# Performance work log

Measured on AMD Instinct MI355X. Metric: run time of the kernel, lower is better.

Reference implementation:

```python
import jax, jax.numpy as jnp
import numpy as np

B, D_IN, D_CTX, UNITS, RANK = 4096, 2048, 512, 2048, 256


def setup_inputs() -> dict:
    key = jax.random.key(0)
    ks = jax.random.split(key, 6)
    scale_u = 1.0 / np.sqrt(D_IN)
    scale_w = 1.0 / np.sqrt(D_CTX)
    return {
        "inputs": jax.random.normal(ks[0], (B, D_IN), dtype=jnp.float32),
        "context": jax.random.normal(ks[1], (B, D_CTX), dtype=jnp.float32),
        "U": jax.random.normal(ks[2], (D_IN, RANK), dtype=jnp.float32) * scale_u,
        "S": jax.random.uniform(ks[3], (RANK,), dtype=jnp.float32) + 0.5,
        "V": jax.random.normal(ks[4], (UNITS, RANK), dtype=jnp.float32) * scale_u,
        "W": jax.random.normal(ks[5], (D_CTX, RANK), dtype=jnp.float32) * scale_w,
        "Bc": jnp.zeros((RANK,), dtype=jnp.float32),
        "bias": jnp.zeros((UNITS,), dtype=jnp.float32),
    }


def reference(inputs, context, U, S, V, W, Bc, bias):
    # h = context @ W + Bc ; chi = sigmoid(h) ; s[b,r] = S[r] * chi[b,r]
    chi = jax.nn.sigmoid(context @ W + Bc)           # [B, R]
    s = S * chi                                       # [B, R]
    # Original math: out[b,m] = sum_{n,r} x[b,n] U[n,r] s[b,r] V[m,r]
    # Reassociated (identical math, no [B,N,M] kernel): ((x @ U) * s) @ V^T
    proj = (inputs @ U) * s                           # [B, R]
    out = proj @ V.T + bias                           # [B, UNITS]
    return out  # activation is linear (None)
```

## Files before the change

kernel.cpp:

```cpp
#include <hip/hip_runtime.h>
#include <math.h>

namespace {

constexpr int Bdim  = 4096;
constexpr int D_IN  = 2048;
constexpr int D_CTX = 512;
constexpr int UNITS = 2048;
constexpr int RANK  = 256;
constexpr int SPLIT = 8;

typedef __bf16 bf16x8 __attribute__((ext_vector_type(8)));
typedef float  f32x4  __attribute__((ext_vector_type(4)));

__global__ __launch_bounds__(256) void k_prep(
    const float* __restrict__ U, const float* __restrict__ W,
    __bf16* __restrict__ Ut, __bf16* __restrict__ Wt) {
  const int job = blockIdx.y;
  const int t = threadIdx.x;
  const float* src = job ? W : U;
  __bf16* dst      = job ? Wt : Ut;
  const int K = job ? D_CTX : D_IN;
  const int tilesK = K / 64;
  const int tid = blockIdx.x;
  if (tid >= tilesK * 4) return;
  const int k0 = (tid % tilesK) * 64;
  const int n0 = (tid / tilesK) * 64;
  __shared__ __bf16 T[64][72];
  const int i  = t >> 4;
  const int j4 = (t & 15) * 4;
  for (int ii = i; ii < 64; ii += 16) {
    float4 v = *(const float4*)(src + (size_t)(k0 + ii) * RANK + n0 + j4);
    T[j4 + 0][ii] = (__bf16)v.x;
    T[j4 + 1][ii] = (__bf16)v.y;
    T[j4 + 2][ii] = (__bf16)v.z;
    T[j4 + 3][ii] = (__bf16)v.w;
  }
  __syncthreads();
  const int jj = t >> 3;
  const int c  = t & 7;
  for (int j2 = jj; j2 < 64; j2 += 32) {
    bf16x8 v = *(const bf16x8*)&T[j2][c * 8];
    *(bf16x8*)(dst + (size_t)(n0 + j2) * K + k0 + c * 8) = v;
  }
}

template <int BM, int BN, int BK, int WAVES_M, int WAVES_N,
          bool A_F32, bool B_F32, int EPI>
__global__ __launch_bounds__(256) void gemm_bt(
    const void* __restrict__ Ap, const void* __restrict__ Btp,
    void* __restrict__ Cp, const float* __restrict__ e0,
    const float* __restrict__ e1, const __bf16* __restrict__ part_in,
    int Mt, int Nt, int Kt, int kchunk) {
  constexpr int FM = BM / WAVES_M / 16;
  constexpr int FN = BN / WAVES_N / 16;
  constexpr int ACH = BM * 8 / 256;
  constexpr int BCH = BN * 8 / 256;
  static_assert(WAVES_M * WAVES_N == 4, "4 waves");
  static_assert(BK == 64, "row = 128B");
  static_assert(ACH >= 1 && BCH >= 1, "chunking");
  static_assert(EPI != 4 || (BM * BN * 4 <= BN * BK * 2), "red fits in Bs");
  __shared__ __align__(16) __bf16 As[BM * BK];
  __shared__ __align__(16) __bf16 Bs[BN * BK];
  const int t  = threadIdx.x;
  const int bm = blockIdx.x * BM;
  const int bn = (EPI == 3) ? 0 : blockIdx.y * BN;
  const int k_lo = (EPI == 3) ? blockIdx.y * kchunk : 0;
  const int k_hi = (EPI == 3) ? k_lo + kchunk : Kt;
  const int w = t >> 6, l = t & 63;
  const int wr0 = (w / WAVES_N) * (FM * 16);
  const int wc0 = (w % WAVES_N) * (FN * 16);
  const int lrow = l & 15;
  const int lk   = l >> 4;
  f32x4 acc[FM][FN] = {};

  float4 a_lo[ACH], a_hi[ACH];
  bf16x8 a_bf[ACH];
  float4 b_lo[BCH], b_hi[BCH];
  bf16x8 b_bf[BCH];

  auto LOADA = [&](int k0) {
#pragma unroll
    for (int ci = 0; ci < ACH; ++ci) {
      const int c = t + ci * 256;
      const int row = c >> 3, kc = c & 7;
      if constexpr (A_F32) {
        const float* g = (const float*)Ap + (size_t)(bm + row) * Kt + k0 + kc * 8;
        a_lo[ci] = *(const float4*)g;
        a_hi[ci] = *(const float4*)(g + 4);
      } else {
        a_bf[ci] = *(const bf16x8*)((const __bf16*)Ap +
                                    (size_t)(bm + row) * Kt + k0 + kc * 8);
      }
    }
  };
  auto LOADB = [&](int k0) {
#pragma unroll
    for (int ci = 0; ci < BCH; ++ci) {
      const int c = t + ci * 256;
      const int row = c >> 3, kc = c & 7;
      if constexpr (B_F32) {
        const float* g = (const float*)Btp + (size_t)(bn + row) * Kt + k0 + kc * 8;
        b_lo[ci] = *(const float4*)g;
        b_hi[ci] = *(const float4*)(g + 4);
      } else {
        b_bf[ci] = *(const bf16x8*)((const __bf16*)Btp +
                                    (size_t)(bn + row) * Kt + k0 + kc * 8);
      }
    }
  };
  auto WRITEA = [&]() {
#pragma unroll
    for (int ci = 0; ci < ACH; ++ci) {
      const int c = t + ci * 256;
      const int row = c >> 3, kc = c & 7;
      bf16x8 v;
      if constexpr (A_F32) {
        v[0] = (__bf16)a_lo[ci].x; v[1] = (__bf16)a_lo[ci].y;
        v[2] = (__bf16)a_lo[ci].z; v[3] = (__bf16)a_lo[ci].w;
        v[4] = (__bf16)a_hi[ci].x; v[5] = (__bf16)a_hi[ci].y;
        v[6] = (__bf16)a_hi[ci].z; v[7] = (__bf16)a_hi[ci].w;
      } else {
        v = a_bf[ci];
      }
      *(bf16x8*)((char*)As + row * 128 + ((kc ^ (row & 7)) * 16)) = v;
    }
  };
  auto WRITEB = [&]() {
#pragma unroll
    for (int ci = 0; ci < BCH; ++ci) {
      const int c = t + ci * 256;
      const int row = c >> 3, kc = c & 7;
      bf16x8 v;
      if constexpr (B_F32) {
        v[0] = (__bf16)b_lo[ci].x; v[1] = (__bf16)b_lo[ci].y;
        v[2] = (__bf16)b_lo[ci].z; v[3] = (__bf16)b_lo[ci].w;
        v[4] = (__bf16)b_hi[ci].x; v[5] = (__bf16)b_hi[ci].y;
        v[6] = (__bf16)b_hi[ci].z; v[7] = (__bf16)b_hi[ci].w;
      } else {
        v = b_bf[ci];
      }
      *(bf16x8*)((char*)Bs + row * 128 + ((kc ^ (row & 7)) * 16)) = v;
    }
  };

  LOADA(k_lo);
  LOADB(k_lo);
  for (int k0 = k_lo; k0 < k_hi; k0 += BK) {
    WRITEA();
    WRITEB();
    __syncthreads();
    if (k0 + BK < k_hi) {
      LOADA(k0 + BK);
      LOADB(k0 + BK);
    }
#pragma unroll
    for (int kk = 0; kk < BK / 32; ++kk) {
      bf16x8 af[FM], bfr[FN];
#pragma unroll
      for (int mf = 0; mf < FM; ++mf) {
        const int row = wr0 + mf * 16 + lrow;
        af[mf] = *(const bf16x8*)((const char*)As + row * 128 +
                                  (((kk * 4 + lk) ^ (row & 7)) * 16));
      }
#pragma unroll
      for (int nf = 0; nf < FN; ++nf) {
        const int row = wc0 + nf * 16 + lrow;
        bfr[nf] = *(const bf16x8*)((const char*)Bs + row * 128 +
                                   (((kk * 4 + lk) ^ (row & 7)) * 16));
      }
#pragma unroll
      for (int mf = 0; mf < FM; ++mf)
#pragma unroll
        for (int nf = 0; nf < FN; ++nf)
          acc[mf][nf] = __builtin_amdgcn_mfma_f32_16x16x32_bf16(
              af[mf], bfr[nf], acc[mf][nf], 0, 0, 0);
    }
    __syncthreads();
  }

  float* red = (float*)Bs;
  if (EPI == 4) {
    const int row = t >> 3;
    const int ch  = (t & 7) * 8;
    float racc[8] = {};
    for (int sl = 0; sl < kchunk; ++sl) {
      bf16x8 v = *(const bf16x8*)(part_in +
                    ((size_t)sl * Mt + bm + row) * Nt + bn + ch);
#pragma unroll
      for (int i = 0; i < 8; ++i) racc[i] += (float)v[i];
    }
#pragma unroll
    for (int i = 0; i < 8; ++i) red[row * BN + ch + i] = racc[i];
    __syncthreads();
  }

#pragma unroll
  for (int mf = 0; mf < FM; ++mf) {
#pragma unroll
    for (int nf = 0; nf < FN; ++nf) {
#pragma unroll
      for (int r = 0; r < 4; ++r) {
        const int lm = wr0 + mf * 16 + lk * 4 + r;
        const int ln = wc0 + nf * 16 + lrow;
        const int m = bm + lm;
        const int n = bn + ln;
        const float val = acc[mf][nf][r];
        if (EPI == 2) {
          ((float*)Cp)[(size_t)m * Nt + n] = val + e0[n];
        } else if (EPI == 3) {
          ((__bf16*)Cp)[(size_t)blockIdx.y * Mt * Nt + (size_t)m * Nt + n] =
              (__bf16)val;
        } else {
          const float h    = val + e1[n];
          const float sval = e0[n] / (1.0f + __expf(-h));
          ((__bf16*)Cp)[(size_t)m * Nt + n] = (__bf16)(red[lm * BN + ln] * sval);
        }
      }
    }
  }
}

}

extern "C" void kernel_launch(void* const* d_in, const int* in_sizes, int n_in,
                              void* d_out, int out_size, void* d_ws, size_t ws_size,
                              hipStream_t stream) {
  const float* inputs  = (const float*)d_in[0];
  const float* context = (const float*)d_in[1];
  const float* U       = (const float*)d_in[2];
  const float* S       = (const float*)d_in[3];
  const float* V       = (const float*)d_in[4];
  const float* W       = (const float*)d_in[5];
  const float* Bc      = (const float*)d_in[6];
  const float* bias    = (const float*)d_in[7];
  float* out = (float*)d_out;

  char* ws = (char*)d_ws;
  __bf16* Ut   = (__bf16*)(ws);
  __bf16* Wt   = (__bf16*)(ws + 1048576);
  __bf16* proj = (__bf16*)(ws + 1310720);
  __bf16* part = (__bf16*)(ws + 3407872);

  k_prep<<<dim3(128, 2), 256, 0, stream>>>(U, W, Ut, Wt);

  gemm_bt<32, 256, 64, 1, 4, true, false, 3>
      <<<dim3(Bdim / 32, SPLIT), 256, 0, stream>>>(
      inputs, Ut, part, nullptr, nullptr, nullptr, Bdim, RANK, D_IN, D_IN / SPLIT);

  gemm_bt<32, 64, 64, 2, 2, true, false, 4>
      <<<dim3(Bdim / 32, RANK / 64), 256, 0, stream>>>(
      context, Wt, proj, S, Bc, part, Bdim, RANK, D_CTX, SPLIT);

  gemm_bt<128, 128, 64, 2, 2, false, true, 2>
      <<<dim3(Bdim / 128, UNITS / 128), 256, 0, stream>>>(
      proj, V, out, bias, nullptr, nullptr, Bdim, UNITS, RANK, 0);
}
```

Measured before the change: 49.73 us.

## Merge gate GEMM into split-K projection launch, add combine kernel, swizzle output tiles

Runs the context gate GEMM (context@W, sigmoid, times S) as an extra grid slice of the split-K projection kernel, so both GEMMs share one launch and execute concurrently. The gate writes s to a bf16 buffer, and a new elementwise kernel sums the split-K partials and multiplies by s to form proj. The output GEMM is specialised and gets a block-index swizzle for better L2 locality. In exchange the change adds an extra s buffer round-trip through memory and uses gate blocks that do 256-wide N tiles.

```diff
diff --git a/kernel.cpp b/kernel.cpp
--- a/kernel.cpp
+++ b/kernel.cpp
@@ -45,102 +45,60 @@
   }
 }
 
-template <int BM, int BN, int BK, int WAVES_M, int WAVES_N,
-          bool A_F32, bool B_F32, int EPI>
-__global__ __launch_bounds__(256) void gemm_bt(
-    const void* __restrict__ Ap, const void* __restrict__ Btp,
-    void* __restrict__ Cp, const float* __restrict__ e0,
-    const float* __restrict__ e1, const __bf16* __restrict__ part_in,
-    int Mt, int Nt, int Kt, int kchunk) {
-  constexpr int FM = BM / WAVES_M / 16;
-  constexpr int FN = BN / WAVES_N / 16;
-  constexpr int ACH = BM * 8 / 256;
-  constexpr int BCH = BN * 8 / 256;
-  static_assert(WAVES_M * WAVES_N == 4, "4 waves");
-  static_assert(BK == 64, "row = 128B");
-  static_assert(ACH >= 1 && BCH >= 1, "chunking");
-  static_assert(EPI != 4 || (BM * BN * 4 <= BN * BK * 2), "red fits in Bs");
+__global__ __launch_bounds__(256) void k_pg(
+    const float* __restrict__ x,   const __bf16* __restrict__ Ut,
+    const float* __restrict__ ctx, const __bf16* __restrict__ Wt,
+    const float* __restrict__ S,   const float* __restrict__ Bc,
+    __bf16* __restrict__ part, __bf16* __restrict__ s_out) {
+  constexpr int BM = 32, BN = 256, BK = 64;
   __shared__ __align__(16) __bf16 As[BM * BK];
   __shared__ __align__(16) __bf16 Bs[BN * BK];
-  const int t  = threadIdx.x;
+  const int t = threadIdx.x;
+  const bool gate = (blockIdx.y == 0);
+  const int slice = (int)blockIdx.y - 1;
   const int bm = blockIdx.x * BM;
-  const int bn = (EPI == 3) ? 0 : blockIdx.y * BN;
-  const int k_lo = (EPI == 3) ? blockIdx.y * kchunk : 0;
-  const int k_hi = (EPI == 3) ? k_lo + kchunk : Kt;
+  const float*  A = gate ? ctx : x;
+  const __bf16* B = gate ? Wt  : Ut;
+  const int Kt   = gate ? D_CTX : D_IN;
+  const int k_lo = gate ? 0 : slice * (D_IN / SPLIT);
+  const int k_hi = gate ? D_CTX : k_lo + (D_IN / SPLIT);
   const int w = t >> 6, l = t & 63;
-  const int wr0 = (w / WAVES_N) * (FM * 16);
-  const int wc0 = (w % WAVES_N) * (FN * 16);
+  const int wc0 = w * 64;
   const int lrow = l & 15;
   const int lk   = l >> 4;
-  f32x4 acc[FM][FN] = {};
-
-  float4 a_lo[ACH], a_hi[ACH];
-  bf16x8 a_bf[ACH];
-  float4 b_lo[BCH], b_hi[BCH];
-  bf16x8 b_bf[BCH];
+  f32x4 acc[2][4] = {};
+
+  float4 a_lo, a_hi;
+  bf16x8 b_bf[8];
+  const int srow = t >> 3, skc = t & 7;
 
   auto LOADA = [&](int k0) {
-#pragma unroll
-    for (int ci = 0; ci < ACH; ++ci) {
-      const int c = t + ci * 256;
-      const int row = c >> 3, kc = c & 7;
-      if constexpr (A_F32) {
-        const float* g = (const float*)Ap + (size_t)(bm + row) * Kt + k0 + kc * 8;
-        a_lo[ci] = *(const float4*)g;
-        a_hi[ci] = *(const float4*)(g + 4);
-      } else {
-        a_bf[ci] = *(const bf16x8*)((const __bf16*)Ap +
-                                    (size_t)(bm + row) * Kt + k0 + kc * 8);
-      }
-    }
+    const float* g = A + (size_t)(bm + srow) * Kt + k0 + skc * 8;
+    a_lo = *(const float4*)g;
+    a_hi = *(const float4*)(g + 4);
   };
   auto LOADB = [&](int k0) {
 #pragma unroll
-    for (int ci = 0; ci < BCH; ++ci) {
-      const int c = t + ci * 256;
-      const int row = c >> 3, kc = c & 7;
-      if constexpr (B_F32) {
-        const float* g = (const float*)Btp + (size_t)(bn + row) * Kt + k0 + kc * 8;
-        b_lo[ci] = *(const float4*)g;
-        b_hi[ci] = *(const float4*)(g + 4);
-      } else {
-        b_bf[ci] = *(const bf16x8*)((const __bf16*)Btp +
-                                    (size_t)(bn + row) * Kt + k0 + kc * 8);
-      }
+    for (int ci = 0; ci < 8; ++ci) {
+      const int c = t + ci * 256;
+      const int row = c >> 3, kc = c & 7;
+      b_bf[ci] = *(const bf16x8*)(B + (size_t)row * Kt + k0 + kc * 8);
     }
   };
   auto WRITEA = [&]() {
-#pragma unroll
-    for (int ci = 0; ci < ACH; ++ci) {
-      const int c = t + ci * 256;
-      const int row = c >> 3, kc = c & 7;
-      bf16x8 v;
-      if constexpr (A_F32) {
-        v[0] = (__bf16)a_lo[ci].x; v[1] = (__bf16)a_lo[ci].y;
-        v[2] = (__bf16)a_lo[ci].z; v[3] = (__bf16)a_lo[ci].w;
-        v[4] = (__bf16)a_hi[ci].x; v[5] = (__bf16)a_hi[ci].y;
-        v[6] = (__bf16)a_hi[ci].z; v[7] = (__bf16)a_hi[ci].w;
-      } else {
-        v = a_bf[ci];
-      }
-      *(bf16x8*)((char*)As + row * 128 + ((kc ^ (row & 7)) * 16)) = v;
-    }
+    bf16x8 v;
+    v[0] = (__bf16)a_lo.x; v[1] = (__bf16)a_lo.y;
+    v[2] = (__bf16)a_lo.z; v[3] = (__bf16)a_lo.w;
+    v[4] = (__bf16)a_hi.x; v[5] = (__bf16)a_hi.y;
+    v[6] = (__bf16)a_hi.z; v[7] = (__bf16)a_hi.w;
+    *(bf16x8*)((char*)As + srow * 128 + ((skc ^ (srow & 7)) * 16)) = v;
   };
   auto WRITEB = [&]() {
 #pragma unroll
-    for (int ci = 0; ci < BCH; ++ci) {
-      const int c = t + ci * 256;
-      const int row = c >> 3, kc = c & 7;
-      bf16x8 v;
-      if constexpr (B_F32) {
-        v[0] = (__bf16)b_lo[ci].x; v[1] = (__bf16)b_lo[ci].y;
-        v[2] = (__bf16)b_lo[ci].z; v[3] = (__bf16)b_lo[ci].w;
-        v[4] = (__bf16)b_hi[ci].x; v[5] = (__bf16)b_hi[ci].y;
-        v[6] = (__bf16)b_hi[ci].z; v[7] = (__bf16)b_hi[ci].w;
-      } else {
-        v = b_bf[ci];
-      }
-      *(bf16x8*)((char*)Bs + row * 128 + ((kc ^ (row & 7)) * 16)) = v;
+    for (int ci = 0; ci < 8; ++ci) {
+      const int c = t + ci * 256;
+      const int row = c >> 3, kc = c & 7;
+      *(bf16x8*)((char*)Bs + row * 128 + ((kc ^ (row & 7)) * 16)) = b_bf[ci];
     }
   };
 
@@ -155,67 +113,174 @@
       LOADB(k0 + BK);
     }
 #pragma unroll
-    for (int kk = 0; kk < BK / 32; ++kk) {
-      bf16x8 af[FM], bfr[FN];
-#pragma unroll
-      for (int mf = 0; mf < FM; ++mf) {
+    for (int kk = 0; kk < 2; ++kk) {
+      bf16x8 af[2], bfr[4];
+#pragma unroll
+      for (int mf = 0; mf < 2; ++mf) {
+        const int row = mf * 16 + lrow;
+        af[mf] = *(const bf16x8*)((const char*)As + row * 128 +
+                                  (((kk * 4 + lk) ^ (row & 7)) * 16));
+      }
+#pragma unroll
+      for (int nf = 0; nf < 4; ++nf) {
+        const int row = wc0 + nf * 16 + lrow;
+        bfr[nf] = *(const bf16x8*)((const char*)Bs + row * 128 +
+                                   (((kk * 4 + lk) ^ (row & 7)) * 16));
+      }
+#pragma unroll
+      for (int mf = 0; mf < 2; ++mf)
+#pragma unroll
+        for (int nf = 0; nf < 4; ++nf)
+          acc[mf][nf] = __builtin_amdgcn_mfma_f32_16x16x32_bf16(
+              af[mf], bfr[nf], acc[mf][nf], 0, 0, 0);
+    }
+    __syncthreads();
+  }
+
+#pragma unroll
+  for (int mf = 0; mf < 2; ++mf) {
+#pragma unroll
+    for (int nf = 0; nf < 4; ++nf) {
+#pragma unroll
+      for (int r = 0; r < 4; ++r) {
+        const int m = bm + mf * 16 + lk * 4 + r;
+        const int n = wc0 + nf * 16 + lrow;
+        const float val = acc[mf][nf][r];
+        if (gate) {
+          const float h = val + Bc[n];
+          s_out[(size_t)m * RANK + n] = (__bf16)(S[n] / (1.0f + __expf(-h)));
+        } else {
+          part[((size_t)slice * Bdim + m) * RANK + n] = (__bf16)val;
+        }
+      }
+    }
+  }
+}
+
+__global__ __launch_bounds__(256) void k_combine(
+    const __bf16* __restrict__ part, const __bf16* __restrict__ s,
+    __bf16* __restrict__ proj) {
+  const size_t i8 = ((size_t)blockIdx.x * 256 + threadIdx.x) * 8;
+  float sum[8] = {};
+#pragma unroll
+  for (int sl = 0; sl < SPLIT; ++sl) {
+    bf16x8 v = *(const bf16x8*)(part + (size_t)sl * Bdim * RANK + i8);
+#pragma unroll
+    for (int i = 0; i < 8; ++i) sum[i] += (float)v[i];
+  }
+  bf16x8 sv = *(const bf16x8*)(s + i8);
+  bf16x8 o;
+#pragma unroll
+  for (int i = 0; i < 8; ++i) o[i] = (__bf16)(sum[i] * (float)sv[i]);
+  *(bf16x8*)(proj + i8) = o;
+}
+
+__global__ __launch_bounds__(256) void k_out(
+    const __bf16* __restrict__ proj, const float* __restrict__ V,
+    const float* __restrict__ bias, float* __restrict__ out) {
+  constexpr int BM = 128, BN = 128, BK = 64;
+  constexpr int Kt = RANK;
+  __shared__ __align__(16) __bf16 As[BM * BK];
+  __shared__ __align__(16) __bf16 Bs[BN * BK];
+  const int t = threadIdx.x;
+  const int lin = (int)(blockIdx.y * gridDim.x + blockIdx.x);
+  const int swz = (lin & 7) * 64 + (lin >> 3);
+  const int bm = (swz & 31) * BM;
+  const int bn = (swz >> 5) * BN;
+  const int w = t >> 6, l = t & 63;
+  const int wr0 = (w >> 1) * 64;
+  const int wc0 = (w & 1) * 64;
+  const int lrow = l & 15;
+  const int lk   = l >> 4;
+  f32x4 acc[4][4] = {};
+
+  bf16x8 a_bf[4];
+  float4 b_lo[4], b_hi[4];
+
+  auto LOADA = [&](int k0) {
+#pragma unroll
+    for (int ci = 0; ci < 4; ++ci) {
+      const int c = t + ci * 256;
+      const int row = c >> 3, kc = c & 7;
+      a_bf[ci] = *(const bf16x8*)(proj + (size_t)(bm + row) * Kt + k0 + kc * 8);
+    }
+  };
+  auto LOADB = [&](int k0) {
+#pragma unroll
+    for (int ci = 0; ci < 4; ++ci) {
+      const int c = t + ci * 256;
+      const int row = c >> 3, kc = c & 7;
+      const float* g = V + (size_t)(bn + row) * Kt + k0 + kc * 8;
+      b_lo[ci] = *(const float4*)g;
+      b_hi[ci] = *(const float4*)(g + 4);
+    }
+  };
+  auto WRITEA = [&]() {
+#pragma unroll
+    for (int ci = 0; ci < 4; ++ci) {
+      const int c = t + ci * 256;
+      const int row = c >> 3, kc = c & 7;
+      *(bf16x8*)((char*)As + row * 128 + ((kc ^ (row & 7)) * 16)) = a_bf[ci];
+    }
+  };
+  auto WRITEB = [&]() {
+#pragma unroll
+    for (int ci = 0; ci < 4; ++ci) {
+      const int c = t + ci * 256;
+      const int row = c >> 3, kc = c & 7;
+      bf16x8 v;
+      v[0] = (__bf16)b_lo[ci].x; v[1] = (__bf16)b_lo[ci].y;
+      v[2] = (__bf16)b_lo[ci].z; v[3] = (__bf16)b_lo[ci].w;
+      v[4] = (__bf16)b_hi[ci].x; v[5] = (__bf16)b_hi[ci].y;
+      v[6] = (__bf16)b_hi[ci].z; v[7] = (__bf16)b_hi[ci].w;
+      *(bf16x8*)((char*)Bs + row * 128 + ((kc ^ (row & 7)) * 16)) = v;
+    }
+  };
+
+  LOADA(0);
+  LOADB(0);
+  for (int k0 = 0; k0 < Kt; k0 += BK) {
+    WRITEA();
+    WRITEB();
+    __syncthreads();
+    if (k0 + BK < Kt) {
+      LOADA(k0 + BK);
+      LOADB(k0 + BK);
+    }
+#pragma unroll
+    for (int kk = 0; kk < 2; ++kk) {
+      bf16x8 af[4], bfr[4];
+#pragma unroll
+      for (int mf = 0; mf < 4; ++mf) {
         const int row = wr0 + mf * 16 + lrow;
         af[mf] = *(const bf16x8*)((const char*)As + row * 128 +
                                   (((kk * 4 + lk) ^ (row & 7)) * 16));
       }
 #pragma unroll
-      for (int nf = 0; nf < FN; ++nf) {
+      for (int nf = 0; nf < 4; ++nf) {
         const int row = wc0 + nf * 16 + lrow;
         bfr[nf] = *(const bf16x8*)((const char*)Bs + row * 128 +
                                    (((kk * 4 + lk) ^ (row & 7)) * 16));
       }
 #pragma unroll
-      for (int mf = 0; mf < FM; ++mf)
-#pragma unroll
-        for (int nf = 0; nf < FN; ++nf)
+      for (int mf = 0; mf < 4; ++mf)
+#pragma unroll
+        for (int nf = 0; nf < 4; ++nf)
           acc[mf][nf] = __builtin_amdgcn_mfma_f32_16x16x32_bf16(
               af[mf], bfr[nf], acc[mf][nf], 0, 0, 0);
     }
     __syncthreads();
   }
 
-  float* red = (float*)Bs;
-  if (EPI == 4) {
-    const int row = t >> 3;
-    const int ch  = (t & 7) * 8;
-    float racc[8] = {};
-    for (int sl = 0; sl < kchunk; ++sl) {
-      bf16x8 v = *(const bf16x8*)(part_in +
-                    ((size_t)sl * Mt + bm + row) * Nt + bn + ch);
-#pragma unroll
-      for (int i = 0; i < 8; ++i) racc[i] += (float)v[i];
-    }
-#pragma unroll
-    for (int i = 0; i < 8; ++i) red[row * BN + ch + i] = racc[i];
-    __syncthreads();
-  }
-
-#pragma unroll
-  for (int mf = 0; mf < FM; ++mf) {
-#pragma unroll
-    for (int nf = 0; nf < FN; ++nf) {
+#pragma unroll
+  for (int mf = 0; mf < 4; ++mf) {
+#pragma unroll
+    for (int nf = 0; nf < 4; ++nf) {
 #pragma unroll
       for (int r = 0; r < 4; ++r) {
-        const int lm = wr0 + mf * 16 + lk * 4 + r;
-        const int ln = wc0 + nf * 16 + lrow;
-        const int m = bm + lm;
-        const int n = bn + ln;
-        const float val = acc[mf][nf][r];
-        if (EPI == 2) {
-          ((float*)Cp)[(size_t)m * Nt + n] = val + e0[n];
-        } else if (EPI == 3) {
-          ((__bf16*)Cp)[(size_t)blockIdx.y * Mt * Nt + (size_t)m * Nt + n] =
-              (__bf16)val;
-        } else {
-          const float h    = val + e1[n];
-          const float sval = e0[n] / (1.0f + __expf(-h));
-          ((__bf16*)Cp)[(size_t)m * Nt + n] = (__bf16)(red[lm * BN + ln] * sval);
-        }
+        const int m = bm + wr0 + mf * 16 + lk * 4 + r;
+        const int n = bn + wc0 + nf * 16 + lrow;
+        out[(size_t)m * UNITS + n] = acc[mf][nf][r] + bias[n];
       }
     }
   }
@@ -240,19 +305,15 @@
   __bf16* Ut   = (__bf16*)(ws);
   __bf16* Wt   = (__bf16*)(ws + 1048576);
   __bf16* proj = (__bf16*)(ws + 1310720);
-  __bf16* part = (__bf16*)(ws + 3407872);
+  __bf16* sbuf = (__bf16*)(ws + 3407872);
+  __bf16* part = (__bf16*)(ws + 5505024);
 
   k_prep<<<dim3(128, 2), 256, 0, stream>>>(U, W, Ut, Wt);
 
-  gemm_bt<32, 256, 64, 1, 4, true, false, 3>
-      <<<dim3(Bdim / 32, SPLIT), 256, 0, stream>>>(
-      inputs, Ut, part, nullptr, nullptr, nullptr, Bdim, RANK, D_IN, D_IN / SPLIT);
-
-  gemm_bt<32, 64, 64, 2, 2, true, false, 4>
-      <<<dim3(Bdim / 32, RANK / 64), 256, 0, stream>>>(
-      context, Wt, proj, S, Bc, part, Bdim, RANK, D_CTX, SPLIT);
-
-  gemm_bt<128, 128, 64, 2, 2, false, true, 2>
-      <<<dim3(Bdim / 128, UNITS / 128), 256, 0, stream>>>(
-      proj, V, out, bias, nullptr, nullptr, Bdim, UNITS, RANK, 0);
-}
+  k_pg<<<dim3(Bdim / 32, SPLIT + 1), 256, 0, stream>>>(
+      inputs, Ut, context, Wt, S, Bc, part, sbuf);
+
+  k_combine<<<dim3((Bdim * RANK) / (256 * 8)), 256, 0, stream>>>(part, sbuf, proj);
+
+  k_out<<<dim3(Bdim / 128, UNITS / 128), 256, 0, stream>>>(proj, V, bias, out);
+}
```

New measurement: 49.00 us. Within noise of the previous version (-1.5%).
